# Kernel optimization log

Hardware: AMD Instinct MI355X
Metric: run time of the kernel (lower is better)

Reference implementation:

```python
import jax, jax.numpy as jnp
import numpy as np

D_MODEL = 1024
HEADS = 16
D_K = D_MODEL // HEADS
D_FF = 4096
B, S = 8, 1024
EPS = 1e-5
NEG = -1e9


def layer_norm(x, g, b):
    mu = jnp.mean(x, axis=-1, keepdims=True)
    var = jnp.var(x, axis=-1, keepdims=True)
    return (x - mu) * jax.lax.rsqrt(var + EPS) * g + b


def setup_inputs() -> dict:
    key = jax.random.key(0)
    ks = jax.random.split(key, 10)
    sc = lambda d: 1.0 / np.sqrt(d)
    return {
        "x": jax.random.normal(ks[0], (B, S, D_MODEL), jnp.float32),
        "mask": jnp.ones((B, 1, 1, S), jnp.int32),
        "wq": jax.random.normal(ks[1], (D_MODEL, D_MODEL), jnp.float32) * sc(D_MODEL),
        "bq": jnp.zeros((D_MODEL,), jnp.float32),
        "wk": jax.random.normal(ks[2], (D_MODEL, D_MODEL), jnp.float32) * sc(D_MODEL),
        "bk": jnp.zeros((D_MODEL,), jnp.float32),
        "wv": jax.random.normal(ks[3], (D_MODEL, D_MODEL), jnp.float32) * sc(D_MODEL),
        "bv": jnp.zeros((D_MODEL,), jnp.float32),
        "wo": jax.random.normal(ks[4], (D_MODEL, D_MODEL), jnp.float32) * sc(D_MODEL),
        "bo": jnp.zeros((D_MODEL,), jnp.float32),
        "w1": jax.random.normal(ks[5], (D_MODEL, D_FF), jnp.float32) * sc(D_MODEL),
        "b1": jnp.zeros((D_FF,), jnp.float32),
        "w2": jax.random.normal(ks[6], (D_FF, D_MODEL), jnp.float32) * sc(D_FF),
        "b2": jnp.zeros((D_MODEL,), jnp.float32),
        "ln1_g": jnp.ones((D_MODEL,), jnp.float32),
        "ln1_b": jnp.zeros((D_MODEL,), jnp.float32),
        "ln2_g": jnp.ones((D_MODEL,), jnp.float32),
        "ln2_b": jnp.zeros((D_MODEL,), jnp.float32),
    }


def reference(x, mask, wq, bq, wk, bk, wv, bv, wo, bo, w1, b1, w2, b2,
              ln1_g, ln1_b, ln2_g, ln2_b):
    b, s, d = x.shape

    # --- self-attention sublayer with residual + LN (pre-norm, dropout=0) ---
    h = layer_norm(x, ln1_g, ln1_b)
    q = (h @ wq + bq).reshape(b, s, HEADS, D_K).transpose(0, 2, 1, 3)  # [b,h,s,dk]
    k = (h @ wk + bk).reshape(b, s, HEADS, D_K).transpose(0, 2, 1, 3)
    v = (h @ wv + bv).reshape(b, s, HEADS, D_K).transpose(0, 2, 1, 3)

    scores = jnp.einsum("bhqd,bhkd->bhqk", q, k) / np.sqrt(D_K)  # [b,h,s,s]
    scores = jnp.where(mask == 0, NEG, scores)
    attn = jax.nn.softmax(scores, axis=-1)
    ctx = jnp.einsum("bhqk,bhkd->bhqd", attn, v)
    ctx = ctx.transpose(0, 2, 1, 3).reshape(b, s, d)
    x = x + (ctx @ wo + bo)

    # --- feed-forward sublayer with residual + LN ---
    h2 = layer_norm(x, ln2_g, ln2_b)
    ff = jax.nn.relu(h2 @ w1 + b1) @ w2 + b2
    return x + ff
```

## Files before the change

### kernel.cpp

```cpp
#include <hip/hip_runtime.h>
#include <hip/hip_bf16.h>

typedef __attribute__((ext_vector_type(8))) __bf16 bf16x8;
typedef __attribute__((ext_vector_type(4))) __bf16 bf16x4;
typedef __attribute__((ext_vector_type(4))) float  f32x4;

__device__ __forceinline__ void gload_lds16(const __bf16* g, __bf16* l) {
    __builtin_amdgcn_global_load_lds(
        (const __attribute__((address_space(1))) void*)g,
        (__attribute__((address_space(3))) void*)l, 16, 0, 0);
}

#define SOFT_BARRIER()                                            \
    do {                                                          \
        asm volatile("s_waitcnt lgkmcnt(0)" ::: "memory");        \
        __builtin_amdgcn_s_barrier();                             \
        asm volatile("" ::: "memory");                            \
    } while (0)

__global__ __launch_bounds__(256) void transpose_all(
    const float* __restrict__ wq, const float* __restrict__ wk,
    const float* __restrict__ wv, const float* __restrict__ wo,
    const float* __restrict__ w1, const float* __restrict__ w2,
    __bf16* __restrict__ wqkvT, __bf16* __restrict__ woT,
    __bf16* __restrict__ w1T, __bf16* __restrict__ w2T,
    const float* __restrict__ bq, const float* __restrict__ bk,
    const float* __restrict__ bv, float* __restrict__ bqkv) {
    __shared__ float t[32][33];
    const int bid = blockIdx.x;
    if (bid >= 12288) {
        const int i = (bid - 12288) * 256 + threadIdx.x;
        bqkv[i] = bq[i]; bqkv[1024 + i] = bk[i]; bqkv[2048 + i] = bv[i];
        return;
    }
    const float* in; __bf16* out; int K, N, nb, kb;
    if (bid < 4096) {
        const int which = bid >> 10, tt = bid & 1023;
        K = 1024; N = 1024;
        in  = which == 0 ? wq : which == 1 ? wk : which == 2 ? wv : wo;
        out = which == 3 ? woT : wqkvT + (size_t)which * 1048576;
        nb = (tt & 31) * 32; kb = (tt >> 5) * 32;
    } else if (bid < 8192) {
        const int tt = bid - 4096;
        in = w1; out = w1T; K = 1024; N = 4096;
        nb = (tt & 127) * 32; kb = (tt >> 7) * 32;
    } else {
        const int tt = bid - 8192;
        in = w2; out = w2T; K = 4096; N = 1024;
        nb = (tt & 31) * 32; kb = (tt >> 5) * 32;
    }
    const int tx = threadIdx.x & 31, ty = threadIdx.x >> 5;
#pragma unroll
    for (int i = 0; i < 32; i += 8)
        t[ty + i][tx] = in[(size_t)(kb + ty + i) * N + nb + tx];
    __syncthreads();
#pragma unroll
    for (int i = 0; i < 32; i += 8)
        out[(size_t)(nb + ty + i) * K + kb + tx] = (__bf16)t[tx][ty + i];
}

__global__ __launch_bounds__(256) void ln_to_bf16(const float* __restrict__ x,
                                                  const float* __restrict__ g,
                                                  const float* __restrict__ bb,
                                                  __bf16* __restrict__ out) {
    const int row = blockIdx.x, t = threadIdx.x;
    const float4 v = ((const float4*)(x + (size_t)row * 1024))[t];
    float s  = v.x + v.y + v.z + v.w;
    float ss = v.x * v.x + v.y * v.y + v.z * v.z + v.w * v.w;
#pragma unroll
    for (int off = 32; off; off >>= 1) {
        s  += __shfl_down(s, off);
        ss += __shfl_down(ss, off);
    }
    __shared__ float ps[4], pss[4];
    if ((t & 63) == 0) { ps[t >> 6] = s; pss[t >> 6] = ss; }
    __syncthreads();
    s  = ps[0] + ps[1] + ps[2] + ps[3];
    ss = pss[0] + pss[1] + pss[2] + pss[3];
    const float mu   = s * (1.0f / 1024.0f);
    const float var  = ss * (1.0f / 1024.0f) - mu * mu;
    const float rinv = rsqrtf(var + 1e-5f);
    const float4 gv = ((const float4*)g)[t];
    const float4 bv = ((const float4*)bb)[t];
    bf16x4 o;
    o[0] = (__bf16)((v.x - mu) * rinv * gv.x + bv.x);
    o[1] = (__bf16)((v.y - mu) * rinv * gv.y + bv.y);
    o[2] = (__bf16)((v.z - mu) * rinv * gv.z + bv.z);
    o[3] = (__bf16)((v.w - mu) * rinv * gv.w + bv.w);
    *(bf16x4*)(out + (size_t)row * 1024 + 4 * t) = o;
}

template <int MODE>
__global__ __launch_bounds__(512, 2) void gemm256(const __bf16* __restrict__ A,
                                                  const __bf16* __restrict__ BT,
                                                  const float* __restrict__ bias,
                                                  __bf16* __restrict__ outp,
                                                  int M, int N, int K, int NMB) {
    __shared__ __align__(16) __bf16 lds[65536];
    const int bid = blockIdx.x;
    const int c8 = bid & 7, loc = bid >> 3;
    const int MH = NMB >> 3;
    const int bm = (c8 * MH + loc % MH) * 256;
    const int bn = (loc / MH) * 256;
    const int tid = threadIdx.x, l = tid & 63, w = tid >> 6;
    const int wm = (w >> 2) * 128, wn = (w & 3) * 64;
    const int lg = l >> 4, lm = l & 15;
    const int NT = K >> 6;

    const __bf16* gsrc[4];
    int ldst[4];
#pragma unroll
    for (int j = 0; j < 4; ++j) {
        const unsigned X = (unsigned)(((j & 1) << 13) + (w << 10) + l * 16);
        const unsigned L = X ^ (((X >> 7) & 7u) << 4);
        const int row = L >> 6, col = (L & 63) >> 1;
        gsrc[j] = (j < 2 ? A + (size_t)(bm + row) * K : BT + (size_t)(bn + row) * K) + col;
        ldst[j] = ((j < 2 ? 0 : 16384) + ((j & 1) << 13) + (w << 10)) >> 1;
    }
    int aoff[2][4], boff[4];
#pragma unroll
    for (int mh = 0; mh < 2; ++mh)
#pragma unroll
        for (int fr = 0; fr < 4; ++fr) {
            const unsigned Lb = (unsigned)(wm + mh * 64 + fr * 16 + lm) * 64 + lg * 16;
            aoff[mh][fr] = (int)(Lb ^ (((Lb >> 7) & 7u) << 4)) >> 1;
        }
#pragma unroll
    for (int n = 0; n < 4; ++n) {
        const unsigned Lb = (unsigned)(wn + n * 16 + lm) * 64 + lg * 16;
        boff[n] = (int)(16384u + (Lb ^ (((Lb >> 7) & 7u) << 4))) >> 1;
    }

    f32x4 acc[8][4];
#pragma unroll
    for (int m = 0; m < 8; ++m)
#pragma unroll
        for (int n = 0; n < 4; ++n) acc[m][n] = f32x4{0.f, 0.f, 0.f, 0.f};

#define ISSUE_SUB(u)                                                          \
    do {                                                                      \
        __bf16* sbp = lds + (((u) & 3) << 14);                                \
        const int go = (u) << 5;                                              \
        _Pragma("unroll")                                                     \
        for (int j = 0; j < 4; ++j) gload_lds16(gsrc[j] + go, sbp + ldst[j]); \
    } while (0)

#define MFMA16(MH_, BREG)                                                     \
    do {                                                                      \
        __builtin_amdgcn_s_setprio(1);                                        \
        _Pragma("unroll")                                                     \
        for (int i = 0; i < 4; ++i)                                           \
            _Pragma("unroll")                                                 \
            for (int n = 0; n < 4; ++n)                                       \
                acc[(MH_)*4 + i][n] = __builtin_amdgcn_mfma_f32_16x16x32_bf16(\
                    af[i], BREG[n], acc[(MH_)*4 + i][n], 0, 0, 0);            \
        __builtin_amdgcn_s_setprio(0);                                        \
    } while (0)

    ISSUE_SUB(0); ISSUE_SUB(1); ISSUE_SUB(2); ISSUE_SUB(3);
    asm volatile("s_waitcnt vmcnt(8)" ::: "memory");
    __builtin_amdgcn_s_barrier();

    for (int t = 0; t < NT; ++t) {
        const int sa = ((2 * t) & 3) << 14, sb = ((2 * t + 1) & 3) << 14;
        bf16x8 af[4], b0[4], b1[4];
#pragma unroll
        for (int fr = 0; fr < 4; ++fr) af[fr] = *(const bf16x8*)(lds + sa + aoff[0][fr]);
#pragma unroll
        for (int n = 0; n < 4; ++n) b0[n] = *(const bf16x8*)(lds + sa + boff[n]);
        asm volatile("" ::: "memory");
        __builtin_amdgcn_s_barrier();
        __builtin_amdgcn_sched_barrier(0);
        MFMA16(0, b0);
        __builtin_amdgcn_sched_barrier(0);
        __builtin_amdgcn_s_barrier();
#pragma unroll
        for (int fr = 0; fr < 4; ++fr) af[fr] = *(const bf16x8*)(lds + sa + aoff[1][fr]);
        asm volatile("" ::: "memory");
        __builtin_amdgcn_s_barrier();
        __builtin_amdgcn_sched_barrier(0);
        MFMA16(1, b0);
        __builtin_amdgcn_sched_barrier(0);
        __builtin_amdgcn_s_barrier();
        if (t < NT - 2) ISSUE_SUB(2 * t + 4);
#pragma unroll
        for (int fr = 0; fr < 4; ++fr) af[fr] = *(const bf16x8*)(lds + sb + aoff[0][fr]);
#pragma unroll
        for (int n = 0; n < 4; ++n) b1[n] = *(const bf16x8*)(lds + sb + boff[n]);
        asm volatile("" ::: "memory");
        __builtin_amdgcn_s_barrier();
        __builtin_amdgcn_sched_barrier(0);
        MFMA16(0, b1);
        __builtin_amdgcn_sched_barrier(0);
        __builtin_amdgcn_s_barrier();
#pragma unroll
        for (int fr = 0; fr < 4; ++fr) af[fr] = *(const bf16x8*)(lds + sb + aoff[1][fr]);
        asm volatile("" ::: "memory");
        __builtin_amdgcn_s_barrier();
        __builtin_amdgcn_sched_barrier(0);
        MFMA16(1, b1);
        __builtin_amdgcn_sched_barrier(0);
        __builtin_amdgcn_s_barrier();
        if (t < NT - 2) {
            ISSUE_SUB(2 * t + 5);
            asm volatile("s_waitcnt vmcnt(8)" ::: "memory");
        } else if (t == NT - 2) {
            asm volatile("s_waitcnt vmcnt(0)" ::: "memory");
        }
        __builtin_amdgcn_s_barrier();
    }
#undef ISSUE_SUB
#undef MFMA16

#pragma unroll
    for (int m = 0; m < 8; ++m) {
        const int row = bm + wm + (m >> 2) * 64 + (m & 3) * 16 + lg * 4;
#pragma unroll
        for (int n = 0; n < 4; ++n) {
            const int col = bn + wn + n * 16 + lm;
            const float bvv = bias[col];
#pragma unroll
            for (int r = 0; r < 4; ++r) {
                const float v = acc[m][n][r] + bvv;
                outp[(size_t)(row + r) * N + col] =
                    (MODE == 1) ? (__bf16)fmaxf(v, 0.f) : (__bf16)v;
            }
        }
    }
}

__global__ __launch_bounds__(512, 2) void gemm256x128(const __bf16* __restrict__ A,
                                                      const __bf16* __restrict__ BT,
                                                      const float* __restrict__ bias,
                                                      const float* __restrict__ resid,
                                                      float* __restrict__ outp,
                                                      int M, int N, int K, int NMB) {
    __shared__ __align__(16) __bf16 lds[49152];
    const int bid = blockIdx.x;
    const int c8 = bid & 7, loc = bid >> 3;
    const int MH = NMB >> 3;
    const int bm = (c8 * MH + loc % MH) * 256;
    const int bn = (loc / MH) * 128;
    const int tid = threadIdx.x, l = tid & 63, w = tid >> 6;
    const int wm = (w >> 1) * 64, wn = (w & 1) * 64;
    const int lg = l >> 4, lm = l & 15;
    const int NT = K >> 6;

    const __bf16* gsrc[3];
    int ldst[3];
#pragma unroll
    for (int j = 0; j < 3; ++j) {
        const unsigned X = (unsigned)((j == 1 ? 8192 : 0) + tid * 16);
        const unsigned L = X ^ (((X >> 7) & 7u) << 4);
        const int row = L >> 6, col = (L & 63) >> 1;
        gsrc[j] = (j < 2 ? A + (size_t)(bm + row) * K : BT + (size_t)(bn + row) * K) + col;
        ldst[j] = ((j < 2 ? (j << 13) : 16384) + (w << 10)) >> 1;
    }
    int aoff[2][2], boff[4];
#pragma unroll
    for (int mh = 0; mh < 2; ++mh)
#pragma unroll
        for (int fr = 0; fr < 2; ++fr) {
            const unsigned Lb = (unsigned)(wm + mh * 32 + fr * 16 + lm) * 64 + lg * 16;
            aoff[mh][fr] = (int)(Lb ^ (((Lb >> 7) & 7u) << 4)) >> 1;
        }
#pragma unroll
    for (int n = 0; n < 4; ++n) {
        const unsigned Lb = (unsigned)(wn + n * 16 + lm) * 64 + lg * 16;
        boff[n] = (int)(16384u + (Lb ^ (((Lb >> 7) & 7u) << 4))) >> 1;
    }

    f32x4 acc[4][4];
#pragma unroll
    for (int m = 0; m < 4; ++m)
#pragma unroll
        for (int n = 0; n < 4; ++n) acc[m][n] = f32x4{0.f, 0.f, 0.f, 0.f};

#define ISSUE_SUB(u)                                                          \
    do {                                                                      \
        __bf16* sbp = lds + ((u) & 3) * 12288;                                \
        const int go = (u) << 5;                                              \
        _Pragma("unroll")                                                     \
        for (int j = 0; j < 3; ++j) gload_lds16(gsrc[j] + go, sbp + ldst[j]); \
    } while (0)

#define MFMA8(MH_, BREG)                                                      \
    do {                                                                      \
        __builtin_amdgcn_s_setprio(1);                                        \
        _Pragma("unroll")                                                     \
        for (int i = 0; i < 2; ++i)                                           \
            _Pragma("unroll")                                                 \
            for (int n = 0; n < 4; ++n)                                       \
                acc[(MH_)*2 + i][n] = __builtin_amdgcn_mfma_f32_16x16x32_bf16(\
                    af[i], BREG[n], acc[(MH_)*2 + i][n], 0, 0, 0);            \
        __builtin_amdgcn_s_setprio(0);                                        \
    } while (0)

    ISSUE_SUB(0); ISSUE_SUB(1); ISSUE_SUB(2); ISSUE_SUB(3);
    asm volatile("s_waitcnt vmcnt(6)" ::: "memory");
    __builtin_amdgcn_s_barrier();

    for (int t = 0; t < NT; ++t) {
        const int sa = ((2 * t) & 3) * 12288, sb = ((2 * t + 1) & 3) * 12288;
        bf16x8 af[2], b0[4], b1[4];
#pragma unroll
        for (int fr = 0; fr < 2; ++fr) af[fr] = *(const bf16x8*)(lds + sa + aoff[0][fr]);
#pragma unroll
        for (int n = 0; n < 4; ++n) b0[n] = *(const bf16x8*)(lds + sa + boff[n]);
        asm volatile("" ::: "memory");
        __builtin_amdgcn_s_barrier();
        __builtin_amdgcn_sched_barrier(0);
        MFMA8(0, b0);
        __builtin_amdgcn_sched_barrier(0);
        __builtin_amdgcn_s_barrier();
#pragma unroll
        for (int fr = 0; fr < 2; ++fr) af[fr] = *(const bf16x8*)(lds + sa + aoff[1][fr]);
        asm volatile("" ::: "memory");
        __builtin_amdgcn_s_barrier();
        __builtin_amdgcn_sched_barrier(0);
        MFMA8(1, b0);
        __builtin_amdgcn_sched_barrier(0);
        __builtin_amdgcn_s_barrier();
        if (t < NT - 2) ISSUE_SUB(2 * t + 4);
#pragma unroll
        for (int fr = 0; fr < 2; ++fr) af[fr] = *(const bf16x8*)(lds + sb + aoff[0][fr]);
#pragma unroll
        for (int n = 0; n < 4; ++n) b1[n] = *(const bf16x8*)(lds + sb + boff[n]);
        asm volatile("" ::: "memory");
        __builtin_amdgcn_s_barrier();
        __builtin_amdgcn_sched_barrier(0);
        MFMA8(0, b1);
        __builtin_amdgcn_sched_barrier(0);
        __builtin_amdgcn_s_barrier();
#pragma unroll
        for (int fr = 0; fr < 2; ++fr) af[fr] = *(const bf16x8*)(lds + sb + aoff[1][fr]);
        asm volatile("" ::: "memory");
        __builtin_amdgcn_s_barrier();
        __builtin_amdgcn_sched_barrier(0);
        MFMA8(1, b1);
        __builtin_amdgcn_sched_barrier(0);
        __builtin_amdgcn_s_barrier();
        if (t < NT - 2) {
            ISSUE_SUB(2 * t + 5);
            asm volatile("s_waitcnt vmcnt(6)" ::: "memory");
        } else if (t == NT - 2) {
            asm volatile("s_waitcnt vmcnt(0)" ::: "memory");
        }
        __builtin_amdgcn_s_barrier();
    }
#undef ISSUE_SUB
#undef MFMA8

#pragma unroll
    for (int m = 0; m < 4; ++m) {
        const int row = bm + wm + m * 16 + lg * 4;
#pragma unroll
        for (int n = 0; n < 4; ++n) {
            const int col = bn + wn + n * 16 + lm;
            const float bvv = bias[col];
#pragma unroll
            for (int r = 0; r < 4; ++r) {
                const size_t idx = (size_t)(row + r) * N + col;
                outp[idx] = resid[idx] + acc[m][n][r] + bvv;
            }
        }
    }
}

__global__ __launch_bounds__(512, 2) void gemm_qkv(const __bf16* __restrict__ A,
                                                   const __bf16* __restrict__ BT,
                                                   const float* __restrict__ bias,
                                                   __bf16* __restrict__ outp,
                                                   __bf16* __restrict__ vTout,
                                                   int M, int N, int K, int NMB) {
    __shared__ __align__(16) __bf16 lds[49152];
    const int bid = blockIdx.x;
    const int c8 = bid & 7, loc = bid >> 3;
    const int MH = NMB >> 3;
    const int bm = (c8 * MH + loc % MH) * 128;
    const int bn = (loc / MH) * 256;
    const int tid = threadIdx.x, l = tid & 63, w = tid >> 6;
    const int wm = (w >> 2) * 64, wn = (w & 3) * 64;
    const int lg = l >> 4, lm = l & 15;
    const int NT = K >> 6;

    const __bf16* gsrc[3];
    int ldst[3];
#pragma unroll
    for (int j = 0; j < 3; ++j) {
        const unsigned X = (unsigned)((j == 0 ? 0 : (j - 1) * 8192) + tid * 16);
        const unsigned L = X ^ (((X >> 7) & 7u) << 4);
        const int row = L >> 6, col = (L & 63) >> 1;
        gsrc[j] = (j == 0 ? A + (size_t)(bm + row) * K : BT + (size_t)(bn + row) * K) + col;
        ldst[j] = ((j == 0 ? 0 : 8192 + (j - 1) * 8192) + (w << 10)) >> 1;
    }
    int aoff[2][2], boff[4];
#pragma unroll
    for (int mh = 0; mh < 2; ++mh)
#pragma unroll
        for (int fr = 0; fr < 2; ++fr) {
            const unsigned Lb = (unsigned)(wm + mh * 32 + fr * 16 + lm) * 64 + lg * 16;
            aoff[mh][fr] = (int)(Lb ^ (((Lb >> 7) & 7u) << 4)) >> 1;
        }
#pragma unroll
    for (int n = 0; n < 4; ++n) {
        const unsigned Lb = (unsigned)(wn + n * 16 + lm) * 64 + lg * 16;
        boff[n] = (int)(8192u + (Lb ^ (((Lb >> 7) & 7u) << 4))) >> 1;
    }

    f32x4 acc[4][4];
#pragma unroll
    for (int m = 0; m < 4; ++m)
#pragma unroll
        for (int n = 0; n < 4; ++n) acc[m][n] = f32x4{0.f, 0.f, 0.f, 0.f};

#define ISSUE_SUB(u)                                                          \
    do {                                                                      \
        __bf16* sbp = lds + ((u) & 3) * 12288;                                \
        const int go = (u) << 5;                                              \
        _Pragma("unroll")                                                     \
        for (int j = 0; j < 3; ++j) gload_lds16(gsrc[j] + go, sbp + ldst[j]); \
    } while (0)

#define PHASE16(SBASE)                                                        \
    do {                                                                      \
        bf16x8 afr[2][2], bfr[4];                                             \
        _Pragma("unroll")                                                     \
        for (int mh = 0; mh < 2; ++mh)                                        \
            _Pragma("unroll")                                                 \
            for (int fr = 0; fr < 2; ++fr)                                    \
                afr[mh][fr] = *(const bf16x8*)(lds + (SBASE) + aoff[mh][fr]); \
        _Pragma("unroll")                                                     \
        for (int n = 0; n < 4; ++n)                                           \
            bfr[n] = *(const bf16x8*)(lds + (SBASE) + boff[n]);               \
        asm volatile("" ::: "memory");                                        \
        __builtin_amdgcn_s_barrier();                                         \
        __builtin_amdgcn_sched_barrier(0);                                    \
        __builtin_amdgcn_s_setprio(1);                                        \
        _Pragma("unroll")                                                     \
        for (int mh = 0; mh < 2; ++mh)                                        \
            _Pragma("unroll")                                                 \
            for (int fr = 0; fr < 2; ++fr)                                    \
                _Pragma("unroll")                                             \
                for (int n = 0; n < 4; ++n)                                   \
                    acc[mh * 2 + fr][n] =                                     \
                        __builtin_amdgcn_mfma_f32_16x16x32_bf16(              \
                            afr[mh][fr], bfr[n], acc[mh * 2 + fr][n], 0, 0, 0);\
        __builtin_amdgcn_s_setprio(0);                                        \
        __builtin_amdgcn_sched_barrier(0);                                    \
        __builtin_amdgcn_s_barrier();                                         \
    } while (0)

    ISSUE_SUB(0); ISSUE_SUB(1); ISSUE_SUB(2); ISSUE_SUB(3);
    asm volatile("s_waitcnt vmcnt(6)" ::: "memory");
    __builtin_amdgcn_s_barrier();

    for (int t = 0; t < NT; ++t) {
        const int sa = ((2 * t) & 3) * 12288, sb = ((2 * t + 1) & 3) * 12288;
        PHASE16(sa);
        if (t < NT - 2) ISSUE_SUB(2 * t + 4);
        PHASE16(sb);
        if (t < NT - 2) {
            ISSUE_SUB(2 * t + 5);
            asm volatile("s_waitcnt vmcnt(6)" ::: "memory");
        } else if (t == NT - 2) {
            asm volatile("s_waitcnt vmcnt(0)" ::: "memory");
        }
        __builtin_amdgcn_s_barrier();
    }
#undef ISSUE_SUB
#undef PHASE16

    const bool isQ = bn < 1024;
#pragma unroll
    for (int m = 0; m < 4; ++m) {
        const int row = bm + wm + m * 16 + lg * 4;
#pragma unroll
        for (int n = 0; n < 4; ++n) {
            const int col = bn + wn + n * 16 + lm;
            const float bvv = bias[col];
            if (bn >= 2048) {
                bf16x4 o;
#pragma unroll
                for (int r = 0; r < 4; ++r) o[r] = (__bf16)(acc[m][n][r] + bvv);
                const int s = row & 1023;
                const int sp = (s & ~31) | (((s >> 2) & 3) << 3) | (((s >> 4) & 1) << 2);
                *(bf16x4*)(vTout + (size_t)((row >> 10) * 1024 + (col - 2048)) * 1024 +
                           sp) = o;
            } else {
#pragma unroll
                for (int r = 0; r < 4; ++r) {
                    float v = acc[m][n][r] + bvv;
                    if (isQ) v *= 0.18033688f;
                    outp[(size_t)(row + r) * 2048 + col] = (__bf16)v;
                }
            }
        }
    }
}

__global__ __launch_bounds__(512, 4) void attn_kernel(const __bf16* __restrict__ qk,
                                                      const __bf16* __restrict__ vT,
                                                      const int* __restrict__ mask,
                                                      __bf16* __restrict__ ctx) {
    const int h = blockIdx.x, qt = blockIdx.y, b = blockIdx.z;
    const int tid = threadIdx.x, w = tid >> 6, l = tid & 63;
    const int lg = l >> 4, lm = l & 15;

    __shared__ __align__(16) __bf16 Ks[2][64][76];
    __shared__ __align__(16) __bf16 Vt[2][64][76];

    const int qrow = qt * 128 + w * 16 + lm;
    const __bf16* qp = qk + (size_t)(b * 1024 + qrow) * 2048 + h * 64 + lg * 8;
    bf16x8 aq[2];
    aq[0] = *(const bf16x8*)qp;
    aq[1] = *(const bf16x8*)(qp + 32);

    const int r0 = tid >> 3, cc0 = (tid & 7) * 8;
    const __bf16* kbase = qk + (size_t)(b * 1024 + r0) * 2048 + 1024 + h * 64 + cc0;
    const __bf16* vbase = vT + (size_t)(b * 1024 + h * 64 + r0) * 1024 + cc0;
    uint4 kreg, vreg;
#define ALOAD(kt)                                                      \
    do {                                                               \
        kreg = *(const uint4*)(kbase + (size_t)(kt) * 131072);         \
        vreg = *(const uint4*)(vbase + (kt) * 64);                     \
    } while (0)
#define AWRITE(bf)                                                     \
    do {                                                               \
        *(uint4*)&Ks[bf][r0][cc0] = kreg;                              \
        *(uint4*)&Vt[bf][r0][cc0] = vreg;                              \
    } while (0)

    ALOAD(0); AWRITE(0); ALOAD(1);
    SOFT_BARRIER();

    const int* mbase = mask + b * 1024;
    float mrun = -1e30f, lsum = 0.f;
    f32x4 oacc[4];
#pragma unroll
    for (int n = 0; n < 4; ++n) oacc[n] = f32x4{0.f, 0.f, 0.f, 0.f};

    for (int kt = 0; kt < 16; ++kt) {
        const int cur = kt & 1;
        if (kt < 15) AWRITE(cur ^ 1);
        if (kt < 14) ALOAD(kt + 2);
        f32x4 sacc[4];
        int4 mk4[4];
#pragma unroll
        for (int n = 0; n < 4; ++n) {
            mk4[n] = *(const int4*)(mbase + kt * 64 + n * 16 + lg * 4);
            sacc[n] = f32x4{0.f, 0.f, 0.f, 0.f};
#pragma unroll
            for (int kk = 0; kk < 2; ++kk) {
                bf16x8 bk = *(const bf16x8*)&Ks[cur][n * 16 + lm][lg * 8 + kk * 32];
                sacc[n] = __builtin_amdgcn_mfma_f32_16x16x32_bf16(bk, aq[kk], sacc[n], 0, 0, 0);
            }
        }
        float p[4][4], mn[4];
#pragma unroll
        for (int n = 0; n < 4; ++n) {
            p[n][0] = mk4[n].x ? sacc[n][0] : -1e9f;
            p[n][1] = mk4[n].y ? sacc[n][1] : -1e9f;
            p[n][2] = mk4[n].z ? sacc[n][2] : -1e9f;
            p[n][3] = mk4[n].w ? sacc[n][3] : -1e9f;
            mn[n] = fmaxf(fmaxf(p[n][0], p[n][1]), fmaxf(p[n][2], p[n][3]));
        }
        float mloc = fmaxf(fmaxf(mn[0], mn[1]), fmaxf(mn[2], mn[3]));
        mloc = fmaxf(mloc, __shfl_xor(mloc, 16));
        mloc = fmaxf(mloc, __shfl_xor(mloc, 32));
        const float pm = fmaxf(mrun, mloc);
        if (!__all(pm - mrun <= 11.5f)) {
            const float sc = exp2f(mrun - pm);
            mrun = pm;
            lsum *= sc;
#pragma unroll
            for (int n = 0; n < 4; ++n)
#pragma unroll
                for (int r = 0; r < 4; ++r) oacc[n][r] *= sc;
        }
        float rsn[4];
#pragma unroll
        for (int n = 0; n < 4; ++n) {
#pragma unroll
            for (int r = 0; r < 4; ++r) p[n][r] = exp2f(p[n][r] - mrun);
            rsn[n] = (p[n][0] + p[n][1]) + (p[n][2] + p[n][3]);
        }
        float rs = (rsn[0] + rsn[1]) + (rsn[2] + rsn[3]);
        rs += __shfl_xor(rs, 16);
        rs += __shfl_xor(rs, 32);
        lsum += rs;
#pragma unroll
        for (int kk = 0; kk < 2; ++kk) {
            bf16x8 pfrag;
#pragma unroll
            for (int r = 0; r < 4; ++r) {
                pfrag[r]     = (__bf16)p[2 * kk][r];
                pfrag[4 + r] = (__bf16)p[2 * kk + 1][r];
            }
#pragma unroll
            for (int nd = 0; nd < 4; ++nd) {
                bf16x8 vf = *(const bf16x8*)&Vt[cur][nd * 16 + lm][lg * 8 + kk * 32];
                oacc[nd] = __builtin_amdgcn_mfma_f32_16x16x32_bf16(vf, pfrag, oacc[nd], 0, 0, 0);
            }
        }
        SOFT_BARRIER();
    }
#undef ALOAD
#undef AWRITE
    const float rinv = 1.0f / lsum;
#pragma unroll
    for (int nd = 0; nd < 4; ++nd) {
        bf16x4 o;
#pragma unroll
        for (int r = 0; r < 4; ++r) o[r] = (__bf16)(oacc[nd][r] * rinv);
        *(bf16x4*)(ctx + (size_t)(b * 1024 + qrow) * 1024 + h * 64 + nd * 16 + lg * 4) = o;
    }
}

extern "C" void kernel_launch(void* const* d_in, const int* in_sizes, int n_in,
                              void* d_out, int out_size, void* d_ws, size_t ws_size,
                              hipStream_t stream) {
    const float* x    = (const float*)d_in[0];
    const int*   mask = (const int*)d_in[1];
    const float* wq   = (const float*)d_in[2];
    const float* bq   = (const float*)d_in[3];
    const float* wk   = (const float*)d_in[4];
    const float* bk   = (const float*)d_in[5];
    const float* wv   = (const float*)d_in[6];
    const float* bv   = (const float*)d_in[7];
    const float* wo   = (const float*)d_in[8];
    const float* bo   = (const float*)d_in[9];
    const float* w1   = (const float*)d_in[10];
    const float* b1   = (const float*)d_in[11];
    const float* w2   = (const float*)d_in[12];
    const float* b2   = (const float*)d_in[13];
    const float* ln1g = (const float*)d_in[14];
    const float* ln1b = (const float*)d_in[15];
    const float* ln2g = (const float*)d_in[16];
    const float* ln2b = (const float*)d_in[17];
    float* out = (float*)d_out;
    char* ws = (char*)d_ws;

    __bf16* wqkvT = (__bf16*)(ws + 0);
    __bf16* woT   = (__bf16*)(ws + 6291456);
    __bf16* w1T   = (__bf16*)(ws + 8388608);
    __bf16* w2T   = (__bf16*)(ws + 16777216);
    float*  bqkv  = (float*)(ws + 25165824);
    __bf16* hb    = (__bf16*)(ws + 25178112);
    __bf16* qkb   = (__bf16*)(ws + 41955328);
    __bf16* vTb   = (__bf16*)(ws + 75509760);
    __bf16* ctxb  = (__bf16*)(ws + 92286976);
    __bf16* ff1b  = qkb;

    transpose_all<<<12292, 256, 0, stream>>>(wq, wk, wv, wo, w1, w2,
                                             wqkvT, woT, w1T, w2T,
                                             bq, bk, bv, bqkv);

    ln_to_bf16<<<8192, 256, 0, stream>>>(x, ln1g, ln1b, hb);
    gemm_qkv<<<768, 512, 0, stream>>>(hb, wqkvT, bqkv, qkb, vTb, 8192, 3072, 1024, 64);
    attn_kernel<<<dim3(16, 8, 8), 512, 0, stream>>>(qkb, vTb, mask, ctxb);
    gemm256x128<<<256, 512, 0, stream>>>(ctxb, woT, bo, x, out, 8192, 1024, 1024, 32);
    ln_to_bf16<<<8192, 256, 0, stream>>>(out, ln2g, ln2b, hb);
    gemm256<1><<<512, 512, 0, stream>>>(hb, w1T, b1, ff1b, 8192, 4096, 1024, 32);
    gemm256x128<<<256, 512, 0, stream>>>(ff1b, w2T, b2, out, out, 8192, 1024, 4096, 32);
}
```

Measured before the change: 363.4 us.

## Restructure residual GEMM to 128-wide K stages with triple-buffered LDS

```diff
diff --git a/kernel.cpp b/kernel.cpp
--- a/kernel.cpp
+++ b/kernel.cpp
@@ -229,13 +229,13 @@
     }
 }
 
-__global__ __launch_bounds__(512, 2) void gemm256x128(const __bf16* __restrict__ A,
+__global__ __launch_bounds__(512, 1) void gemm256x128(const __bf16* __restrict__ A,
                                                       const __bf16* __restrict__ BT,
                                                       const float* __restrict__ bias,
                                                       const float* __restrict__ resid,
                                                       float* __restrict__ outp,
                                                       int M, int N, int K, int NMB) {
-    __shared__ __align__(16) __bf16 lds[49152];
+    __shared__ __align__(16) __bf16 lds[73728];
     const int bid = blockIdx.x;
     const int c8 = bid & 7, loc = bid >> 3;
     const int MH = NMB >> 3;
@@ -244,31 +244,36 @@
     const int tid = threadIdx.x, l = tid & 63, w = tid >> 6;
     const int wm = (w >> 1) * 64, wn = (w & 1) * 64;
     const int lg = l >> 4, lm = l & 15;
-    const int NT = K >> 6;
-
-    const __bf16* gsrc[3];
-    int ldst[3];
-#pragma unroll
-    for (int j = 0; j < 3; ++j) {
-        const unsigned X = (unsigned)((j == 1 ? 8192 : 0) + tid * 16);
+    const int NU = K >> 6;
+
+    const __bf16* gsrc[6];
+    int ldst[6];
+#pragma unroll
+    for (int j = 0; j < 6; ++j) {
+        const unsigned X = (unsigned)((j < 4 ? j * 8192 : (j - 4) * 8192) + tid * 16);
         const unsigned L = X ^ (((X >> 7) & 7u) << 4);
-        const int row = L >> 6, col = (L & 63) >> 1;
-        gsrc[j] = (j < 2 ? A + (size_t)(bm + row) * K : BT + (size_t)(bn + row) * K) + col;
-        ldst[j] = ((j < 2 ? (j << 13) : 16384) + (w << 10)) >> 1;
-    }
-    int aoff[2][2], boff[4];
+        const int row = L >> 7, col = (L & 127) >> 1;
+        gsrc[j] = (j < 4 ? A + (size_t)(bm + row) * K : BT + (size_t)(bn + row) * K) + col;
+        ldst[j] = ((j < 4 ? j * 8192 : 32768 + (j - 4) * 8192) + (w << 10)) >> 1;
+    }
+    int aoff[2][2][2], boff[4][2];
 #pragma unroll
     for (int mh = 0; mh < 2; ++mh)
 #pragma unroll
-        for (int fr = 0; fr < 2; ++fr) {
-            const unsigned Lb = (unsigned)(wm + mh * 32 + fr * 16 + lm) * 64 + lg * 16;
-            aoff[mh][fr] = (int)(Lb ^ (((Lb >> 7) & 7u) << 4)) >> 1;
-        }
-#pragma unroll
-    for (int n = 0; n < 4; ++n) {
-        const unsigned Lb = (unsigned)(wn + n * 16 + lm) * 64 + lg * 16;
-        boff[n] = (int)(16384u + (Lb ^ (((Lb >> 7) & 7u) << 4))) >> 1;
-    }
+        for (int fr = 0; fr < 2; ++fr)
+#pragma unroll
+            for (int kk = 0; kk < 2; ++kk) {
+                const unsigned Lb = (unsigned)(wm + mh * 32 + fr * 16 + lm) * 128 +
+                                    kk * 64 + lg * 16;
+                aoff[mh][fr][kk] = (int)(Lb ^ (((Lb >> 7) & 7u) << 4)) >> 1;
+            }
+#pragma unroll
+    for (int n = 0; n < 4; ++n)
+#pragma unroll
+        for (int kk = 0; kk < 2; ++kk) {
+            const unsigned Lb = (unsigned)(wn + n * 16 + lm) * 128 + kk * 64 + lg * 16;
+            boff[n][kk] = (int)(32768u + (Lb ^ (((Lb >> 7) & 7u) << 4))) >> 1;
+        }
 
     f32x4 acc[4][4];
 #pragma unroll
@@ -276,80 +281,61 @@
 #pragma unroll
         for (int n = 0; n < 4; ++n) acc[m][n] = f32x4{0.f, 0.f, 0.f, 0.f};
 
-#define ISSUE_SUB(u)                                                          \
+#define ISSUE_SUB(u, base)                                                    \
     do {                                                                      \
-        __bf16* sbp = lds + ((u) & 3) * 12288;                                \
-        const int go = (u) << 5;                                              \
+        const int go = (u) << 6;                                              \
         _Pragma("unroll")                                                     \
-        for (int j = 0; j < 3; ++j) gload_lds16(gsrc[j] + go, sbp + ldst[j]); \
-    } while (0)
-
-#define MFMA8(MH_, BREG)                                                      \
-    do {                                                                      \
-        __builtin_amdgcn_s_setprio(1);                                        \
-        _Pragma("unroll")                                                     \
-        for (int i = 0; i < 2; ++i)                                           \
-            _Pragma("unroll")                                                 \
-            for (int n = 0; n < 4; ++n)                                       \
-                acc[(MH_)*2 + i][n] = __builtin_amdgcn_mfma_f32_16x16x32_bf16(\
-                    af[i], BREG[n], acc[(MH_)*2 + i][n], 0, 0, 0);            \
-        __builtin_amdgcn_s_setprio(0);                                        \
-    } while (0)
-
-    ISSUE_SUB(0); ISSUE_SUB(1); ISSUE_SUB(2); ISSUE_SUB(3);
+        for (int j = 0; j < 6; ++j)                                           \
+            gload_lds16(gsrc[j] + go, lds + (base) + ldst[j]);                \
+    } while (0)
+
+    ISSUE_SUB(0, 0); ISSUE_SUB(1, 24576);
     asm volatile("s_waitcnt vmcnt(6)" ::: "memory");
     __builtin_amdgcn_s_barrier();
 
-    for (int t = 0; t < NT; ++t) {
-        const int sa = ((2 * t) & 3) * 12288, sb = ((2 * t + 1) & 3) * 12288;
-        bf16x8 af[2], b0[4], b1[4];
-#pragma unroll
-        for (int fr = 0; fr < 2; ++fr) af[fr] = *(const bf16x8*)(lds + sa + aoff[0][fr]);
-#pragma unroll
-        for (int n = 0; n < 4; ++n) b0[n] = *(const bf16x8*)(lds + sa + boff[n]);
+    int bo = 0;
+    for (int u = 0; u < NU; ++u) {
+        bf16x8 afr[2][2][2], bfr[4][2];
+#pragma unroll
+        for (int mh = 0; mh < 2; ++mh)
+#pragma unroll
+            for (int fr = 0; fr < 2; ++fr)
+#pragma unroll
+                for (int kk = 0; kk < 2; ++kk)
+                    afr[mh][fr][kk] = *(const bf16x8*)(lds + bo + aoff[mh][fr][kk]);
+#pragma unroll
+        for (int n = 0; n < 4; ++n)
+#pragma unroll
+            for (int kk = 0; kk < 2; ++kk)
+                bfr[n][kk] = *(const bf16x8*)(lds + bo + boff[n][kk]);
         asm volatile("" ::: "memory");
         __builtin_amdgcn_s_barrier();
         __builtin_amdgcn_sched_barrier(0);
-        MFMA8(0, b0);
-        __builtin_amdgcn_sched_barrier(0);
-        __builtin_amdgcn_s_barrier();
-#pragma unroll
-        for (int fr = 0; fr < 2; ++fr) af[fr] = *(const bf16x8*)(lds + sa + aoff[1][fr]);
-        asm volatile("" ::: "memory");
-        __builtin_amdgcn_s_barrier();
-        __builtin_amdgcn_sched_barrier(0);
-        MFMA8(1, b0);
-        __builtin_amdgcn_sched_barrier(0);
-        __builtin_amdgcn_s_barrier();
-        if (t < NT - 2) ISSUE_SUB(2 * t + 4);
-#pragma unroll
-        for (int fr = 0; fr < 2; ++fr) af[fr] = *(const bf16x8*)(lds + sb + aoff[0][fr]);
-#pragma unroll
-        for (int n = 0; n < 4; ++n) b1[n] = *(const bf16x8*)(lds + sb + boff[n]);
-        asm volatile("" ::: "memory");
-        __builtin_amdgcn_s_barrier();
-        __builtin_amdgcn_sched_barrier(0);
-        MFMA8(0, b1);
-        __builtin_amdgcn_sched_barrier(0);
-        __builtin_amdgcn_s_barrier();
-#pragma unroll
-        for (int fr = 0; fr < 2; ++fr) af[fr] = *(const bf16x8*)(lds + sb + aoff[1][fr]);
-        asm volatile("" ::: "memory");
-        __builtin_amdgcn_s_barrier();
-        __builtin_amdgcn_sched_barrier(0);
-        MFMA8(1, b1);
-        __builtin_amdgcn_sched_barrier(0);
-        __builtin_amdgcn_s_barrier();
-        if (t < NT - 2) {
-            ISSUE_SUB(2 * t + 5);
+        __builtin_amdgcn_s_setprio(1);
+#pragma unroll
+        for (int kk = 0; kk < 2; ++kk)
+#pragma unroll
+            for (int mh = 0; mh < 2; ++mh)
+#pragma unroll
+                for (int fr = 0; fr < 2; ++fr)
+#pragma unroll
+                    for (int n = 0; n < 4; ++n)
+                        acc[mh * 2 + fr][n] = __builtin_amdgcn_mfma_f32_16x16x32_bf16(
+                            afr[mh][fr][kk], bfr[n][kk], acc[mh * 2 + fr][n], 0, 0, 0);
+        __builtin_amdgcn_s_setprio(0);
+        __builtin_amdgcn_sched_barrier(0);
+        __builtin_amdgcn_s_barrier();
+        if (u + 2 < NU) {
+            int bs = bo + 49152; if (bs >= 73728) bs -= 73728;
+            ISSUE_SUB(u + 2, bs);
             asm volatile("s_waitcnt vmcnt(6)" ::: "memory");
-        } else if (t == NT - 2) {
+        } else {
             asm volatile("s_waitcnt vmcnt(0)" ::: "memory");
         }
         __builtin_amdgcn_s_barrier();
+        bo += 24576; if (bo == 73728) bo = 0;
     }
 #undef ISSUE_SUB
-#undef MFMA8
 
 #pragma unroll
     for (int m = 0; m < 4; ++m) {
```

New measurement: 366.5 us. Within noise of the previous version (+0.8%).
